# Kernel optimization log

Measured on AMD Instinct MI355X. Metric: run time of the kernel, lower is better.

Reference implementation:

```python
import jax, jax.numpy as jnp
import numpy as np


def setup_inputs() -> dict:
    key = jax.random.key(0)
    k1, k2, k3 = jax.random.split(key, 3)
    N, P, C = 4, 1024, 3
    H, W = 128, 128
    # coordinates in pixel space: x in [0, W), y in [0, H)
    coords01 = jax.random.uniform(k1, (N, P, 2), dtype=jnp.float32)
    coordinates = coords01 * jnp.array([W, H], dtype=jnp.float32)
    values = jax.random.normal(k2, (N, P, C), dtype=jnp.float32)
    # sigma in [1.0, 3.0), one std per batch element
    sigma = 1.0 + 2.0 * jax.random.uniform(k3, (N, 1), dtype=jnp.float32)
    return {
        "coordinates": coordinates,
        "values": values,
        "sigma": sigma,
        "height": H,
        "width": W,
    }


def reference(coordinates, values, sigma, height, width):
    # coordinates: [N, P, 2] (x, y); values: [N, P, C]; sigma: [N, 1]
    dt = coordinates.dtype
    ys = jnp.arange(height, dtype=dt)  # [H]
    xs = jnp.arange(width, dtype=dt)   # [W]
    x = coordinates[..., 0]            # [N, P]
    y = coordinates[..., 1]            # [N, P]
    # squared distance from each point to each grid cell: [N, P, H, W]
    dy2 = (ys[None, None, :, None] - y[:, :, None, None]) ** 2  # [N,P,H,1]
    dx2 = (xs[None, None, None, :] - x[:, :, None, None]) ** 2  # [N,P,1,W]
    dist2 = dy2 + dx2                                           # [N,P,H,W]
    inv_two_sigma2 = 0.5 / (sigma ** 2)                         # [N,1]
    weight = jnp.exp(-dist2 * inv_two_sigma2[:, :, None, None])  # [N,P,H,W]
    # scatter-add each point's gaussian-weighted value onto the grid
    out = jnp.einsum('nphw,npc->nchw', weight, values)  # [N,C,H,W]
    return out
```

## Files before the change

kernel.cpp:

```cpp
#include <hip/hip_runtime.h>
#include <hip/hip_bf16.h>


#define BLOCK 256
#define SEGS  8

__device__ __forceinline__ float fast_exp2(float x) {
#if __has_builtin(__builtin_amdgcn_exp2f)
    return __builtin_amdgcn_exp2f(x);
#else
    return exp2f(x);
#endif
}

__global__ __launch_bounds__(BLOCK) void splat2d_gather_seg(
    const float* __restrict__ coords,
    const float* __restrict__ vals,
    const float* __restrict__ sigma,
    const int*   __restrict__ wptr,
    float*       __restrict__ out,
    int P, int pixPerN, int blocksPerN, int nSeg)
{
    const int W = *wptr;
    int t = blockIdx.x;
    const int seg = t % nSeg;  t /= nSeg;
    const int n   = t / blocksPerN;
    const int blk = t % blocksPerN;

    const int pix = blk * BLOCK + threadIdx.x;
    const int h = pix / W;
    const int w = pix - h * W;

    const float fx = (float)w;
    const float fy = (float)h;

    const float sg = sigma[n];
    const float negInv2 = -1.44269504088896f * 0.5f / (sg * sg);

    const int PS = P / nSeg;
    const int p0 = seg * PS;
    const float* __restrict__ cp = coords + ((size_t)n * P + p0) * 2;
    const float* __restrict__ vp = vals   + ((size_t)n * P + p0) * 3;

    float a0 = 0.f, a1 = 0.f, a2 = 0.f;

#pragma unroll 8
    for (int p = 0; p < PS; ++p) {
        const float x = cp[2 * p + 0];
        const float y = cp[2 * p + 1];
        const float dx = fx - x;
        const float dy = fy - y;
        const float d2 = fmaf(dx, dx, dy * dy);
        const float wgt = fast_exp2(d2 * negInv2);
        a0 = fmaf(wgt, vp[3 * p + 0], a0);
        a1 = fmaf(wgt, vp[3 * p + 1], a1);
        a2 = fmaf(wgt, vp[3 * p + 2], a2);
    }

    const size_t base = ((size_t)n * 3) * (size_t)pixPerN + (size_t)pix;
    unsafeAtomicAdd(&out[base],                       a0);
    unsafeAtomicAdd(&out[base + (size_t)pixPerN],     a1);
    unsafeAtomicAdd(&out[base + 2 * (size_t)pixPerN], a2);
}

extern "C" void kernel_launch(void* const* d_in, const int* in_sizes, int n_in,
                              void* d_out, int out_size, void* d_ws, size_t ws_size,
                              hipStream_t stream) {
    const float* coords = (const float*)d_in[0];
    const float* vals   = (const float*)d_in[1];
    const float* sigma  = (const float*)d_in[2];
    const int* wptr = (const int*)d_in[4];

    const int N = in_sizes[2];
    const int P = in_sizes[0] / (2 * N);
    const int C = in_sizes[1] / (N * P);
    const int pixPerN = out_size / (N * C);

    float* out = (float*)d_out;

    const int nSeg = (P % SEGS == 0) ? SEGS : 1;
    const int blocksPerN = pixPerN / BLOCK;
    const int grid = N * blocksPerN * nSeg;

    hipMemsetAsync(out, 0, (size_t)out_size * sizeof(float), stream);

    splat2d_gather_seg<<<grid, BLOCK, 0, stream>>>(coords, vals, sigma, wptr,
                                                   out, P, pixPerN, blocksPerN, nSeg);
}
```

Baseline: 80.54 us.

## Stage points in LDS and expand squared distance into precomputed FMA form

Each block now loads its segment of points into shared memory once, packed as float4+float2 with a precomputed s*(x^2+y^2) term. The inner loop expands the squared distance algebraically, so the exponent becomes two FMAs plus an add per point using per-pixel constants. This removes per-thread global/scalar loads and a few ALU ops per point. The cost is a barrier and LDS reads, plus possible precision loss from the expanded distance form when pixel and point coordinates are large. The nSeg=1 fallback path would overflow the shared buffer when P exceeds 128, which is only guarded for P<=1024 with 8 segments.

```diff
diff --git a/kernel.cpp b/kernel.cpp
--- a/kernel.cpp
+++ b/kernel.cpp
@@ -13,7 +13,7 @@
 #endif
 }
 
-__global__ __launch_bounds__(BLOCK) void splat2d_gather_seg(
+__global__ __launch_bounds__(BLOCK) void splat2d_lds(
     const float* __restrict__ coords,
     const float* __restrict__ vals,
     const float* __restrict__ sigma,
@@ -21,40 +21,56 @@
     float*       __restrict__ out,
     int P, int pixPerN, int blocksPerN, int nSeg)
 {
+    const int PS_MAX = 1024;
+    __shared__ float4 ptA[PS_MAX / SEGS];
+    __shared__ float2 ptB[PS_MAX / SEGS];
+
     const int W = *wptr;
     int t = blockIdx.x;
     const int seg = t % nSeg;  t /= nSeg;
     const int n   = t / blocksPerN;
     const int blk = t % blocksPerN;
 
-    const int pix = blk * BLOCK + threadIdx.x;
-    const int h = pix / W;
-    const int w = pix - h * W;
-
-    const float fx = (float)w;
-    const float fy = (float)h;
-
     const float sg = sigma[n];
-    const float negInv2 = -1.44269504088896f * 0.5f / (sg * sg);
+    const float s  = -1.44269504088896f * 0.5f / (sg * sg);
 
     const int PS = P / nSeg;
     const int p0 = seg * PS;
     const float* __restrict__ cp = coords + ((size_t)n * P + p0) * 2;
     const float* __restrict__ vp = vals   + ((size_t)n * P + p0) * 3;
 
+    for (int p = threadIdx.x; p < PS; p += BLOCK) {
+        const float x  = cp[2 * p + 0];
+        const float y  = cp[2 * p + 1];
+        const float v0 = vp[3 * p + 0];
+        const float v1 = vp[3 * p + 1];
+        const float v2 = vp[3 * p + 2];
+        const float c  = s * fmaf(x, x, y * y);
+        ptA[p] = make_float4(x, y, c, v0);
+        ptB[p] = make_float2(v1, v2);
+    }
+    __syncthreads();
+
+    const int pix = blk * BLOCK + threadIdx.x;
+    const int h = pix / W;
+    const int w = pix - h * W;
+    const float fx = (float)w;
+    const float fy = (float)h;
+    const float tx = -2.0f * s * fx;
+    const float ty = -2.0f * s * fy;
+    const float bb = s * fmaf(fx, fx, fy * fy);
+
     float a0 = 0.f, a1 = 0.f, a2 = 0.f;
 
 #pragma unroll 8
     for (int p = 0; p < PS; ++p) {
-        const float x = cp[2 * p + 0];
-        const float y = cp[2 * p + 1];
-        const float dx = fx - x;
-        const float dy = fy - y;
-        const float d2 = fmaf(dx, dx, dy * dy);
-        const float wgt = fast_exp2(d2 * negInv2);
-        a0 = fmaf(wgt, vp[3 * p + 0], a0);
-        a1 = fmaf(wgt, vp[3 * p + 1], a1);
-        a2 = fmaf(wgt, vp[3 * p + 2], a2);
+        const float4 q = ptA[p];
+        const float2 r = ptB[p];
+        const float e = fmaf(tx, q.x, fmaf(ty, q.y, bb + q.z));
+        const float wgt = fast_exp2(e);
+        a0 = fmaf(wgt, q.w, a0);
+        a1 = fmaf(wgt, r.x, a1);
+        a2 = fmaf(wgt, r.y, a2);
     }
 
     const size_t base = ((size_t)n * 3) * (size_t)pixPerN + (size_t)pix;
@@ -78,12 +94,12 @@
 
     float* out = (float*)d_out;
 
-    const int nSeg = (P % SEGS == 0) ? SEGS : 1;
+    const int nSeg = (P % SEGS == 0 && P <= 1024) ? SEGS : 1;
     const int blocksPerN = pixPerN / BLOCK;
     const int grid = N * blocksPerN * nSeg;
 
     hipMemsetAsync(out, 0, (size_t)out_size * sizeof(float), stream);
 
-    splat2d_gather_seg<<<grid, BLOCK, 0, stream>>>(coords, vals, sigma, wptr,
-                                                   out, P, pixPerN, blocksPerN, nSeg);
+    splat2d_lds<<<grid, BLOCK, 0, stream>>>(coords, vals, sigma, wptr,
+                                            out, P, pixPerN, blocksPerN, nSeg);
 }
```

Result: faster. 75.85 us (-5.8%).
